# Performance work log

Measured on AMD Instinct MI355X. Metric: run time of the kernel, lower is better.

## Reference

```python
import jax, jax.numpy as jnp
import numpy as np

H, W = 96, 96
NUM_ITERS = 5          # num_iterations from __init__
SXY_G, COMPAT_G = 3.0, 3.0    # addPairwiseGaussian(sxy=(3,3), compat=3)
SXY_B, SRGB, COMPAT_B = 50.0, 20.0, 10.0  # addPairwiseBilateral(sxy=50, srgb=20, compat=10)
EPS = 1e-8


def _crf_marginals(img, m):
    """Exact dense mean-field CRF (the math pydensecrf approximates via
    permutohedral lattice). img: [H,W] float, m: [H,W] int in {0,1}.
    Returns Q: [2, N] marginals."""
    Hh, Ww = img.shape
    N = Hh * Ww
    # --- unary (replicates the source exactly, including the label swap) ---
    onehot0 = (m == 0).astype(jnp.float32)
    unary_p = jnp.stack([1.0 - onehot0, onehot0]).reshape(2, -1)   # [2, N]
    unary = -jnp.log(jnp.clip(unary_p, EPS, 1.0))
    # --- pairwise kernel: 3 * gaussian + 10 * bilateral, self-excluded ---
    ys, xs = jnp.meshgrid(jnp.arange(Hh, dtype=jnp.float32),
                          jnp.arange(Ww, dtype=jnp.float32), indexing='ij')
    pos = jnp.stack([xs.ravel(), ys.ravel()], axis=-1)             # [N, 2]
    f = img.reshape(-1)                                            # [N]
    d2 = jnp.sum((pos[:, None, :] - pos[None, :, :]) ** 2, axis=-1)  # [N, N] spatial sq dist
    # grayscale image duplicated into 2 feature channels -> 2 * (f_i - f_j)^2
    df2 = 2.0 * (f[:, None] - f[None, :]) ** 2                     # [N, N]
    K = (COMPAT_G * jnp.exp(-d2 / (2.0 * SXY_G ** 2))
         + COMPAT_B * jnp.exp(-d2 / (2.0 * SXY_B ** 2) - df2 / (2.0 * SRGB ** 2)))
    idx = jnp.arange(N)
    K = K.at[idx, idx].set(0.0)  # exclude self-interaction
    # --- mean-field iterations (Potts compatibility, 2 labels) ---
    Q = jax.nn.softmax(-unary, axis=0)  # [2, N]
    for _ in range(NUM_ITERS):
        msg = Q @ K                     # [2, N]; K is symmetric
        pairwise = msg[::-1]            # Potts: penalty from the OTHER label
        Q = jax.nn.softmax(-unary - pairwise, axis=0)
    return Q


def setup_inputs() -> dict:
    key = jax.random.key(0)
    k1, k2 = jax.random.split(key)
    image = jax.random.uniform(k1, (1, 1, H, W), dtype=jnp.float32) * 255.0
    mask = jax.random.randint(k2, (1, 1, H, W), 0, 2)
    return {"image": image, "mask": mask}


def reference(image, mask):
    img = image[0, 0]
    m = mask[0, 0]
    Q = _crf_marginals(img, m)
    pred = jnp.argmax(Q, axis=0).reshape(img.shape)
    return pred[None, None].astype(jnp.float32)   # [1,1,H,W]
```

## Files before the change

### kernel.cpp

```cpp
#include <hip/hip_runtime.h>

constexpr int W    = 96;
constexpr int NPIX = 9216;
constexpr int NM   = 23;
constexpr int NPKB = 12;
constexpr int NP   = 13;

constexpr float LCLIP = 18.420681f;
constexpr float KTH   = 0.0174532925f;
constexpr float ACOEF = 1.9693944f;
constexpr float ADC   = 0.9846972f;
constexpr float AEXP  = 0.0304617f;

__global__ __launch_bounds__(256) void k_init(const float* __restrict__ img,
                                              float4* __restrict__ B4){
    int px = blockIdx.x*256 + threadIdx.x;
    float th = img[px] * KTH;
    float c[48];
    c[0] = 1.f; c[47] = 0.f;
    float s1, c1;
    sincosf(th, &s1, &c1);
    float cm = 1.f, sm = 0.f;
    #pragma unroll
    for (int m = 1; m <= NM; ++m){
        float cn = cm*c1 - sm*s1;
        float sn = sm*c1 + cm*s1;
        cm = cn; sm = sn;
        c[m]    = cm;
        c[NM+m] = sm;
    }
    #pragma unroll
    for (int p = 0; p < NPKB; ++p)
        B4[(size_t)p*NPIX + px] = make_float4(c[4*p], c[4*p+1], c[4*p+2], c[4*p+3]);
}

template<int MODE>
__global__ __launch_bounds__(384) void k_H(const int* __restrict__ mask,
        const float4* __restrict__ B4,
        const float* __restrict__ partV, const float* __restrict__ partVk,
        float* __restrict__ ksum, const float* __restrict__ qprev, float* __restrict__ qcur,
        float4* __restrict__ H4T, float* __restrict__ H3T,
        float4* __restrict__ H4Tk, float* __restrict__ H3Tk)
{
    __shared__ float4 P4[8*97];
    __shared__ float  qp[8*97];
    __shared__ float  tw[193];
    const int  t    = threadIdx.x;
    const int  B    = blockIdx.x;
    const int  g0   = blockIdx.y;
    const bool ones = (MODE==0) && (g0 >= NP);
    const int  pack = ones ? g0 - NP : g0;
    const bool G3   = (pack == NPKB);

    if (t < 193){
        float d = (float)(t - 96);
        tw[t] = G3 ? __expf(-d*d*(1.f/18.f)) : __expf(-d*d*(1.f/5000.f));
    }
    float A[4];
    if (!G3){
        #pragma unroll
        for (int jj = 0; jj < 4; ++jj){
            int ch = 4*pack + jj;
            if (ch == 0)       A[jj] = ADC;
            else if (ch <= 46){
                int m = (ch <= NM) ? ch : ch - NM;
                A[jj] = ACOEF * __expf(-AEXP*(float)(m*m));
            } else             A[jj] = 0.f;
        }
    }

    #pragma unroll
    for (int k = 0; k < 2; ++k){
        int l  = t + k*384;
        int px = B*768 + l;
        float q;
        if (ones){
            q = 1.f;
        } else if (MODE == 0){
            q = (mask[px]==0) ? 1.f/(1.f+__expf( LCLIP)) : 1.f/(1.f+__expf(-LCLIP));
        } else {
            float m = 0.f;
            #pragma unroll
            for (int p = 0; p < NP; ++p) m += partV[(size_t)p*NPIX + px];
            float kk;
            if (MODE == 1){
                kk = 0.f;
                #pragma unroll
                for (int p = 0; p < NP; ++p) kk += partVk[(size_t)p*NPIX + px];
                kk -= 13.f;
                if (g0 == 0) ksum[px] = kk;
            } else {
                kk = ksum[px];
            }
            float duv = (mask[px]==0) ? LCLIP : -LCLIP;
            float delta = duv + kk - 2.f*(m - 13.f*qprev[px]);
            q = 1.f/(1.f+__expf(delta));
        }
        if (!ones && g0 == 0) qcur[px] = q;
        int ryl = l/96, xx = l - ryl*96;
        if (!G3){
            float4 b = B4[(size_t)pack*NPIX + px];
            P4[ryl*97 + xx] = make_float4(q*A[0]*b.x, q*A[1]*b.y, q*A[2]*b.z, q*A[3]*b.w);
        } else {
            qp[ryl*97 + xx] = q;
        }
    }
    __syncthreads();

    const int r = t & 7, xg = t >> 3;
    const int y = 8*B + r;
    if (!G3){
        float4 a0 = make_float4(0.f,0.f,0.f,0.f), a1 = a0;
        #pragma unroll 4
        for (int xp = 0; xp < W; ++xp){
            float4 v  = P4[r*97 + xp];
            float  w0 = tw[xg - xp + 96];
            float  w1 = tw[xg - xp + 96 + 48];
            a0.x = fmaf(w0,v.x,a0.x); a0.y = fmaf(w0,v.y,a0.y);
            a0.z = fmaf(w0,v.z,a0.z); a0.w = fmaf(w0,v.w,a0.w);
            a1.x = fmaf(w1,v.x,a1.x); a1.y = fmaf(w1,v.y,a1.y);
            a1.z = fmaf(w1,v.z,a1.z); a1.w = fmaf(w1,v.w,a1.w);
        }
        float4* dst = ones ? H4Tk : H4T;
        dst[(size_t)pack*NPIX + xg*W      + y] = a0;
        dst[(size_t)pack*NPIX + (xg+48)*W + y] = a1;
    } else {
        float h0 = 0.f, h1 = 0.f;
        #pragma unroll 4
        for (int xp = 0; xp < W; ++xp){
            float qv = qp[r*97 + xp];
            h0 = fmaf(tw[xg - xp + 96],      qv, h0);
            h1 = fmaf(tw[xg - xp + 96 + 48], qv, h1);
        }
        float* dg = ones ? H3Tk : H3T;
        dg[xg*W + y] = h0; dg[(xg+48)*W + y] = h1;
    }
}

__global__ __launch_bounds__(384) void k_V(const float4* __restrict__ B4,
        const float4* __restrict__ H4T, const float4* __restrict__ H4Tk,
        const float* __restrict__ H3T, const float* __restrict__ H3Tk,
        float* __restrict__ partV, float* __restrict__ partVk)
{
    __shared__ float4 Hl[8*97];
    __shared__ float  Hl3[8*97];
    __shared__ float  tw[193];
    const int  t    = threadIdx.x;
    const int  C    = blockIdx.x;
    const int  g0   = blockIdx.y;
    const bool ones = g0 >= NP;
    const int  pack = ones ? g0 - NP : g0;
    const bool G3   = (pack == NPKB);

    if (t < 193){
        float d = (float)(t - 96);
        tw[t] = G3 ? __expf(-d*d*(1.f/18.f)) : __expf(-d*d*(1.f/5000.f));
    }
    #pragma unroll
    for (int k = 0; k < 2; ++k){
        int l = t + k*384;
        int col = l/96, yy = l - col*96;
        if (!G3) Hl[col*97 + yy]  = (ones ? H4Tk : H4T)[(size_t)pack*NPIX + (8*C+col)*W + yy];
        else     Hl3[col*97 + yy] = (ones ? H3Tk : H3T)[(8*C+col)*W + yy];
    }
    __syncthreads();

    const int r = t & 7, yg = t >> 3;
    const int x = 8*C + r;
    if (!G3){
        float4 a0 = make_float4(0.f,0.f,0.f,0.f), a1 = a0;
        #pragma unroll 4
        for (int yp = 0; yp < W; ++yp){
            float4 v  = Hl[r*97 + yp];
            float  w0 = tw[yg - yp + 96];
            float  w1 = tw[yg - yp + 96 + 48];
            a0.x = fmaf(w0,v.x,a0.x); a0.y = fmaf(w0,v.y,a0.y);
            a0.z = fmaf(w0,v.z,a0.z); a0.w = fmaf(w0,v.w,a0.w);
            a1.x = fmaf(w1,v.x,a1.x); a1.y = fmaf(w1,v.y,a1.y);
            a1.z = fmaf(w1,v.z,a1.z); a1.w = fmaf(w1,v.w,a1.w);
        }
        int px0 = yg*W + x, px1 = (yg+48)*W + x;
        float4 b0 = B4[(size_t)pack*NPIX + px0];
        float4 b1 = B4[(size_t)pack*NPIX + px1];
        float* dst = ones ? partVk : partV;
        dst[(size_t)pack*NPIX + px0] = a0.x*b0.x + a0.y*b0.y + a0.z*b0.z + a0.w*b0.w;
        dst[(size_t)pack*NPIX + px1] = a1.x*b1.x + a1.y*b1.y + a1.z*b1.z + a1.w*b1.w;
    } else {
        float h0 = 0.f, h1 = 0.f;
        #pragma unroll 4
        for (int yp = 0; yp < W; ++yp){
            float v = Hl3[r*97 + yp];
            h0 = fmaf(tw[yg - yp + 96],      v, h0);
            h1 = fmaf(tw[yg - yp + 96 + 48], v, h1);
        }
        float* dst = ones ? partVk : partV;
        dst[(size_t)pack*NPIX + yg*W + x]      = 3.f*h0;
        dst[(size_t)pack*NPIX + (yg+48)*W + x] = 3.f*h1;
    }
}

__global__ __launch_bounds__(256) void k_F(const int* __restrict__ mask,
        const float* __restrict__ partV, const float* __restrict__ ksum,
        const float* __restrict__ qprev, float* __restrict__ out){
    int px = blockIdx.x*256 + threadIdx.x;
    float m = 0.f;
    #pragma unroll
    for (int p = 0; p < NP; ++p) m += partV[(size_t)p*NPIX + px];
    float duv = (mask[px]==0) ? LCLIP : -LCLIP;
    float delta = duv + ksum[px] - 2.f*(m - 13.f*qprev[px]);
    out[px] = (delta > 0.f) ? 1.f : 0.f;
}

extern "C" void kernel_launch(void* const* d_in, const int* in_sizes, int n_in,
                              void* d_out, int out_size, void* d_ws, size_t ws_size,
                              hipStream_t stream){
    const float* img  = (const float*)d_in[0];
    const int*   mask = (const int*)d_in[1];
    float* out = (float*)d_out;
    float* ws  = (float*)d_ws;

    constexpr size_t TBL = (size_t)NPKB*NPIX*4;
    float4* B4    = (float4*)ws;
    float4* H4T   = (float4*)(ws + TBL);
    float4* H4Tk  = (float4*)(ws + 2*TBL);
    float*  base  = ws + 3*TBL;
    float* H3T   = base;
    float* H3Tk  = H3T  + NPIX;
    float* partV = H3Tk + NPIX;
    float* partVk= partV + (size_t)NP*NPIX;
    float* qA    = partVk + (size_t)NP*NPIX;
    float* qB    = qA + NPIX;
    float* ksum  = qB + NPIX;

    dim3 b(384);
    k_init<<<dim3(36), dim3(256), 0, stream>>>(img, B4);
    k_H<0><<<dim3(12,2*NP), b, 0, stream>>>(mask, B4, partV, partVk, ksum, qA, qA, H4T, H3T, H4Tk, H3Tk);
    k_V   <<<dim3(12,2*NP), b, 0, stream>>>(B4, H4T, H4Tk, H3T, H3Tk, partV, partVk);
    k_H<1><<<dim3(12,NP), b, 0, stream>>>(mask, B4, partV, partVk, ksum, qA, qB, H4T, H3T, H4Tk, H3Tk);
    k_V   <<<dim3(12,NP), b, 0, stream>>>(B4, H4T, H4Tk, H3T, H3Tk, partV, partVk);
    k_H<2><<<dim3(12,NP), b, 0, stream>>>(mask, B4, partV, partVk, ksum, qB, qA, H4T, H3T, H4Tk, H3Tk);
    k_V   <<<dim3(12,NP), b, 0, stream>>>(B4, H4T, H4Tk, H3T, H3Tk, partV, partVk);
    k_H<2><<<dim3(12,NP), b, 0, stream>>>(mask, B4, partV, partVk, ksum, qA, qB, H4T, H3T, H4Tk, H3Tk);
    k_V   <<<dim3(12,NP), b, 0, stream>>>(B4, H4T, H4Tk, H3T, H3Tk, partV, partVk);
    k_H<2><<<dim3(12,NP), b, 0, stream>>>(mask, B4, partV, partVk, ksum, qB, qA, H4T, H3T, H4Tk, H3Tk);
    k_V   <<<dim3(12,NP), b, 0, stream>>>(B4, H4T, H4Tk, H3T, H3Tk, partV, partVk);
    k_F<<<dim3(36), dim3(256), 0, stream>>>(mask, partV, ksum, qA, out);
}
```

Baseline: 76.51 us.

## Split separable convolution reduction dimension into four quarters across blocks

```diff
diff --git a/kernel.cpp b/kernel.cpp
--- a/kernel.cpp
+++ b/kernel.cpp
@@ -5,6 +5,9 @@
 constexpr int NM   = 23;
 constexpr int NPKB = 12;
 constexpr int NP   = 13;
+constexpr int NSPL = 4;
+constexpr int QW   = 24;
+constexpr int NPL  = NSPL*NP;
 
 constexpr float LCLIP = 18.420681f;
 constexpr float KTH   = 0.0174532925f;
@@ -42,11 +45,12 @@
         float4* __restrict__ H4T, float* __restrict__ H3T,
         float4* __restrict__ H4Tk, float* __restrict__ H3Tk)
 {
-    __shared__ float4 P4[8*97];
-    __shared__ float  qp[8*97];
+    __shared__ float4 P4[8][QW+1];
+    __shared__ float  qp[8][QW+1];
     __shared__ float  tw[193];
     const int  t    = threadIdx.x;
-    const int  B    = blockIdx.x;
+    const int  B    = blockIdx.x >> 2;
+    const int  q    = blockIdx.x & 3;
     const int  g0   = blockIdx.y;
     const bool ones = (MODE==0) && (g0 >= NP);
     const int  pack = ones ? g0 - NP : g0;
@@ -69,24 +73,23 @@
         }
     }
 
-    #pragma unroll
-    for (int k = 0; k < 2; ++k){
-        int l  = t + k*384;
-        int px = B*768 + l;
-        float q;
+    if (t < 192){
+        int ryl = t / QW, xx = t - ryl*QW;
+        int px  = (8*B + ryl)*W + q*QW + xx;
+        float qv;
         if (ones){
-            q = 1.f;
+            qv = 1.f;
         } else if (MODE == 0){
-            q = (mask[px]==0) ? 1.f/(1.f+__expf( LCLIP)) : 1.f/(1.f+__expf(-LCLIP));
+            qv = (mask[px]==0) ? 1.f/(1.f+__expf( LCLIP)) : 1.f/(1.f+__expf(-LCLIP));
         } else {
             float m = 0.f;
             #pragma unroll
-            for (int p = 0; p < NP; ++p) m += partV[(size_t)p*NPIX + px];
+            for (int p = 0; p < NPL; ++p) m += partV[(size_t)p*NPIX + px];
             float kk;
             if (MODE == 1){
                 kk = 0.f;
                 #pragma unroll
-                for (int p = 0; p < NP; ++p) kk += partVk[(size_t)p*NPIX + px];
+                for (int p = 0; p < NPL; ++p) kk += partVk[(size_t)p*NPIX + px];
                 kk -= 13.f;
                 if (g0 == 0) ksum[px] = kk;
             } else {
@@ -94,45 +97,45 @@
             }
             float duv = (mask[px]==0) ? LCLIP : -LCLIP;
             float delta = duv + kk - 2.f*(m - 13.f*qprev[px]);
-            q = 1.f/(1.f+__expf(delta));
-        }
-        if (!ones && g0 == 0) qcur[px] = q;
-        int ryl = l/96, xx = l - ryl*96;
+            qv = 1.f/(1.f+__expf(delta));
+        }
+        if (!ones && g0 == 0) qcur[px] = qv;
         if (!G3){
             float4 b = B4[(size_t)pack*NPIX + px];
-            P4[ryl*97 + xx] = make_float4(q*A[0]*b.x, q*A[1]*b.y, q*A[2]*b.z, q*A[3]*b.w);
+            P4[ryl][xx] = make_float4(qv*A[0]*b.x, qv*A[1]*b.y, qv*A[2]*b.z, qv*A[3]*b.w);
         } else {
-            qp[ryl*97 + xx] = q;
+            qp[ryl][xx] = qv;
         }
     }
     __syncthreads();
 
     const int r = t & 7, xg = t >> 3;
     const int y = 8*B + r;
+    const int ib = xg - q*QW + 96;
     if (!G3){
         float4 a0 = make_float4(0.f,0.f,0.f,0.f), a1 = a0;
         #pragma unroll 4
-        for (int xp = 0; xp < W; ++xp){
-            float4 v  = P4[r*97 + xp];
-            float  w0 = tw[xg - xp + 96];
-            float  w1 = tw[xg - xp + 96 + 48];
+        for (int k = 0; k < QW; ++k){
+            float4 v  = P4[r][k];
+            float  w0 = tw[ib - k];
+            float  w1 = tw[ib - k + 48];
             a0.x = fmaf(w0,v.x,a0.x); a0.y = fmaf(w0,v.y,a0.y);
             a0.z = fmaf(w0,v.z,a0.z); a0.w = fmaf(w0,v.w,a0.w);
             a1.x = fmaf(w1,v.x,a1.x); a1.y = fmaf(w1,v.y,a1.y);
             a1.z = fmaf(w1,v.z,a1.z); a1.w = fmaf(w1,v.w,a1.w);
         }
-        float4* dst = ones ? H4Tk : H4T;
-        dst[(size_t)pack*NPIX + xg*W      + y] = a0;
-        dst[(size_t)pack*NPIX + (xg+48)*W + y] = a1;
+        float4* dst = (ones ? H4Tk : H4T) + (size_t)(q*NPKB + pack)*NPIX;
+        dst[xg*W      + y] = a0;
+        dst[(xg+48)*W + y] = a1;
     } else {
         float h0 = 0.f, h1 = 0.f;
         #pragma unroll 4
-        for (int xp = 0; xp < W; ++xp){
-            float qv = qp[r*97 + xp];
-            h0 = fmaf(tw[xg - xp + 96],      qv, h0);
-            h1 = fmaf(tw[xg - xp + 96 + 48], qv, h1);
-        }
-        float* dg = ones ? H3Tk : H3T;
+        for (int k = 0; k < QW; ++k){
+            float qv = qp[r][k];
+            h0 = fmaf(tw[ib - k],      qv, h0);
+            h1 = fmaf(tw[ib - k + 48], qv, h1);
+        }
+        float* dg = (ones ? H3Tk : H3T) + (size_t)q*NPIX;
         dg[xg*W + y] = h0; dg[(xg+48)*W + y] = h1;
     }
 }
@@ -142,11 +145,12 @@
         const float* __restrict__ H3T, const float* __restrict__ H3Tk,
         float* __restrict__ partV, float* __restrict__ partVk)
 {
-    __shared__ float4 Hl[8*97];
-    __shared__ float  Hl3[8*97];
+    __shared__ float4 Hl[8][QW+1];
+    __shared__ float  Hl3[8][QW+1];
     __shared__ float  tw[193];
     const int  t    = threadIdx.x;
-    const int  C    = blockIdx.x;
+    const int  C    = blockIdx.x >> 2;
+    const int  qv   = blockIdx.x & 3;
     const int  g0   = blockIdx.y;
     const bool ones = g0 >= NP;
     const int  pack = ones ? g0 - NP : g0;
@@ -156,24 +160,39 @@
         float d = (float)(t - 96);
         tw[t] = G3 ? __expf(-d*d*(1.f/18.f)) : __expf(-d*d*(1.f/5000.f));
     }
-    #pragma unroll
-    for (int k = 0; k < 2; ++k){
-        int l = t + k*384;
-        int col = l/96, yy = l - col*96;
-        if (!G3) Hl[col*97 + yy]  = (ones ? H4Tk : H4T)[(size_t)pack*NPIX + (8*C+col)*W + yy];
-        else     Hl3[col*97 + yy] = (ones ? H3Tk : H3T)[(8*C+col)*W + yy];
+    if (t < 192){
+        int col = t / QW, yy = t - col*QW;
+        int off = (8*C + col)*W + qv*QW + yy;
+        if (!G3){
+            float4 s = make_float4(0.f,0.f,0.f,0.f);
+            const float4* src = ones ? H4Tk : H4T;
+            #pragma unroll
+            for (int hq = 0; hq < NSPL; ++hq){
+                float4 v = src[(size_t)(hq*NPKB + pack)*NPIX + off];
+                s.x += v.x; s.y += v.y; s.z += v.z; s.w += v.w;
+            }
+            Hl[col][yy] = s;
+        } else {
+            float s = 0.f;
+            const float* src = ones ? H3Tk : H3T;
+            #pragma unroll
+            for (int hq = 0; hq < NSPL; ++hq) s += src[(size_t)hq*NPIX + off];
+            Hl3[col][yy] = s;
+        }
     }
     __syncthreads();
 
     const int r = t & 7, yg = t >> 3;
-    const int x = 8*C + r;
+    const int x  = 8*C + r;
+    const int ib = yg - qv*QW + 96;
+    float* dst = (ones ? partVk : partV) + (size_t)(qv*NP + pack)*NPIX;
     if (!G3){
         float4 a0 = make_float4(0.f,0.f,0.f,0.f), a1 = a0;
         #pragma unroll 4
-        for (int yp = 0; yp < W; ++yp){
-            float4 v  = Hl[r*97 + yp];
-            float  w0 = tw[yg - yp + 96];
-            float  w1 = tw[yg - yp + 96 + 48];
+        for (int k = 0; k < QW; ++k){
+            float4 v  = Hl[r][k];
+            float  w0 = tw[ib - k];
+            float  w1 = tw[ib - k + 48];
             a0.x = fmaf(w0,v.x,a0.x); a0.y = fmaf(w0,v.y,a0.y);
             a0.z = fmaf(w0,v.z,a0.z); a0.w = fmaf(w0,v.w,a0.w);
             a1.x = fmaf(w1,v.x,a1.x); a1.y = fmaf(w1,v.y,a1.y);
@@ -182,20 +201,18 @@
         int px0 = yg*W + x, px1 = (yg+48)*W + x;
         float4 b0 = B4[(size_t)pack*NPIX + px0];
         float4 b1 = B4[(size_t)pack*NPIX + px1];
-        float* dst = ones ? partVk : partV;
-        dst[(size_t)pack*NPIX + px0] = a0.x*b0.x + a0.y*b0.y + a0.z*b0.z + a0.w*b0.w;
-        dst[(size_t)pack*NPIX + px1] = a1.x*b1.x + a1.y*b1.y + a1.z*b1.z + a1.w*b1.w;
+        dst[px0] = a0.x*b0.x + a0.y*b0.y + a0.z*b0.z + a0.w*b0.w;
+        dst[px1] = a1.x*b1.x + a1.y*b1.y + a1.z*b1.z + a1.w*b1.w;
     } else {
         float h0 = 0.f, h1 = 0.f;
         #pragma unroll 4
-        for (int yp = 0; yp < W; ++yp){
-            float v = Hl3[r*97 + yp];
-            h0 = fmaf(tw[yg - yp + 96],      v, h0);
-            h1 = fmaf(tw[yg - yp + 96 + 48], v, h1);
-        }
-        float* dst = ones ? partVk : partV;
-        dst[(size_t)pack*NPIX + yg*W + x]      = 3.f*h0;
-        dst[(size_t)pack*NPIX + (yg+48)*W + x] = 3.f*h1;
+        for (int k = 0; k < QW; ++k){
+            float v = Hl3[r][k];
+            h0 = fmaf(tw[ib - k],      v, h0);
+            h1 = fmaf(tw[ib - k + 48], v, h1);
+        }
+        dst[yg*W + x]      = 3.f*h0;
+        dst[(yg+48)*W + x] = 3.f*h1;
     }
 }
 
@@ -205,7 +222,7 @@
     int px = blockIdx.x*256 + threadIdx.x;
     float m = 0.f;
     #pragma unroll
-    for (int p = 0; p < NP; ++p) m += partV[(size_t)p*NPIX + px];
+    for (int p = 0; p < NPL; ++p) m += partV[(size_t)p*NPIX + px];
     float duv = (mask[px]==0) ? LCLIP : -LCLIP;
     float delta = duv + ksum[px] - 2.f*(m - 13.f*qprev[px]);
     out[px] = (delta > 0.f) ? 1.f : 0.f;
@@ -219,30 +236,31 @@
     float* out = (float*)d_out;
     float* ws  = (float*)d_ws;
 
-    constexpr size_t TBL = (size_t)NPKB*NPIX*4;
+    constexpr size_t TBL  = (size_t)NPKB*NPIX*4;
+    constexpr size_t HSZ  = (size_t)NSPL*NPKB*NPIX*4;
     float4* B4    = (float4*)ws;
     float4* H4T   = (float4*)(ws + TBL);
-    float4* H4Tk  = (float4*)(ws + 2*TBL);
-    float*  base  = ws + 3*TBL;
+    float4* H4Tk  = (float4*)(ws + TBL + HSZ);
+    float*  base  = ws + TBL + 2*HSZ;
     float* H3T   = base;
-    float* H3Tk  = H3T  + NPIX;
-    float* partV = H3Tk + NPIX;
-    float* partVk= partV + (size_t)NP*NPIX;
-    float* qA    = partVk + (size_t)NP*NPIX;
+    float* H3Tk  = H3T  + (size_t)NSPL*NPIX;
+    float* partV = H3Tk + (size_t)NSPL*NPIX;
+    float* partVk= partV + (size_t)NPL*NPIX;
+    float* qA    = partVk + (size_t)NPL*NPIX;
     float* qB    = qA + NPIX;
     float* ksum  = qB + NPIX;
 
     dim3 b(384);
     k_init<<<dim3(36), dim3(256), 0, stream>>>(img, B4);
-    k_H<0><<<dim3(12,2*NP), b, 0, stream>>>(mask, B4, partV, partVk, ksum, qA, qA, H4T, H3T, H4Tk, H3Tk);
-    k_V   <<<dim3(12,2*NP), b, 0, stream>>>(B4, H4T, H4Tk, H3T, H3Tk, partV, partVk);
-    k_H<1><<<dim3(12,NP), b, 0, stream>>>(mask, B4, partV, partVk, ksum, qA, qB, H4T, H3T, H4Tk, H3Tk);
-    k_V   <<<dim3(12,NP), b, 0, stream>>>(B4, H4T, H4Tk, H3T, H3Tk, partV, partVk);
-    k_H<2><<<dim3(12,NP), b, 0, stream>>>(mask, B4, partV, partVk, ksum, qB, qA, H4T, H3T, H4Tk, H3Tk);
-    k_V   <<<dim3(12,NP), b, 0, stream>>>(B4, H4T, H4Tk, H3T, H3Tk, partV, partVk);
-    k_H<2><<<dim3(12,NP), b, 0, stream>>>(mask, B4, partV, partVk, ksum, qA, qB, H4T, H3T, H4Tk, H3Tk);
-    k_V   <<<dim3(12,NP), b, 0, stream>>>(B4, H4T, H4Tk, H3T, H3Tk, partV, partVk);
-    k_H<2><<<dim3(12,NP), b, 0, stream>>>(mask, B4, partV, partVk, ksum, qB, qA, H4T, H3T, H4Tk, H3Tk);
-    k_V   <<<dim3(12,NP), b, 0, stream>>>(B4, H4T, H4Tk, H3T, H3Tk, partV, partVk);
+    k_H<0><<<dim3(48,2*NP), b, 0, stream>>>(mask, B4, partV, partVk, ksum, qA, qA, H4T, H3T, H4Tk, H3Tk);
+    k_V   <<<dim3(48,2*NP), b, 0, stream>>>(B4, H4T, H4Tk, H3T, H3Tk, partV, partVk);
+    k_H<1><<<dim3(48,NP), b, 0, stream>>>(mask, B4, partV, partVk, ksum, qA, qB, H4T, H3T, H4Tk, H3Tk);
+    k_V   <<<dim3(48,NP), b, 0, stream>>>(B4, H4T, H4Tk, H3T, H3Tk, partV, partVk);
+    k_H<2><<<dim3(48,NP), b, 0, stream>>>(mask, B4, partV, partVk, ksum, qB, qA, H4T, H3T, H4Tk, H3Tk);
+    k_V   <<<dim3(48,NP), b, 0, stream>>>(B4, H4T, H4Tk, H3T, H3Tk, partV, partVk);
+    k_H<2><<<dim3(48,NP), b, 0, stream>>>(mask, B4, partV, partVk, ksum, qA, qB, H4T, H3T, H4Tk, H3Tk);
+    k_V   <<<dim3(48,NP), b, 0, stream>>>(B4, H4T, H4Tk, H3T, H3Tk, partV, partVk);
+    k_H<2><<<dim3(48,NP), b, 0, stream>>>(mask, B4, partV, partVk, ksum, qB, qA, H4T, H3T, H4Tk, H3Tk);
+    k_V   <<<dim3(48,NP), b, 0, stream>>>(B4, H4T, H4Tk, H3T, H3Tk, partV, partVk);
     k_F<<<dim3(36), dim3(256), 0, stream>>>(mask, partV, ksum, qA, out);
 }
```

Result: slower. 100.1 us (+30.8%).
